# Performance work log

Hardware: AMD Instinct MI355X
Metric: run time of the kernel (lower is better)

Reference implementation:

```python
import jax, jax.numpy as jnp
import numpy as np
from jax import lax

N = 100000
G = 256          # voxel grid extent per axis
MULT = 8
C_HID = 32 * MULT  # 256
K3 = 27


def setup_inputs() -> dict:
    key = jax.random.key(0)
    k_feat, k1, k2, k3, k4 = jax.random.split(key, 5)
    # unique voxel coordinates in a G^3 grid (sparse tensors have no duplicate coords)
    rng = np.random.default_rng(0)
    lin = rng.choice(G * G * G, size=N, replace=False)
    coords = np.stack([lin // (G * G), (lin // G) % G, lin % G], axis=1).astype(np.int32)
    feats = jax.random.normal(k_feat, (N, 2), dtype=jnp.float32)
    def w(k, cin, cout):
        return jax.random.normal(k, (K3, cin, cout), dtype=jnp.float32) / np.sqrt(K3 * cin)
    return {
        "coords": jnp.asarray(coords),
        "feats": feats,
        "W1": w(k1, 2, C_HID),
        "W2": w(k2, C_HID, C_HID),
        "W3": w(k3, C_HID, C_HID),
        "W4": w(k4, C_HID, 2),
    }


def _neighbor_map(coords):
    """Kernel map for a 3x3x3 stride-1 sparse conv: for each of 27 offsets and each
    point i, the index j of the point at coords[i]+offset (and a validity mask).
    Built once and shared by all four layers (stride=1 preserves coordinates)."""
    S = G + 2  # pad linearization base so offsets in {-1,0,1} never wrap
    c = coords.astype(jnp.int32) + 1
    keys = (c[:, 0] * S + c[:, 1]) * S + c[:, 2]            # [N]
    order = jnp.argsort(keys)
    skeys = keys[order]
    offs = jnp.array([[dx, dy, dz] for dx in (-1, 0, 1)
                      for dy in (-1, 0, 1) for dz in (-1, 0, 1)], dtype=jnp.int32)  # [27,3]
    nc = c[None, :, :] + offs[:, None, :]                    # [27,N,3]
    qk = (nc[..., 0] * S + nc[..., 1]) * S + nc[..., 2]      # [27,N]
    pos = jnp.clip(jnp.searchsorted(skeys, qk), 0, N - 1)
    valid = skeys[pos] == qk                                 # [27,N]
    idx = order[pos]                                         # [27,N]
    return idx, valid


def _sparse_conv(feats, W, idx, valid):
    """gather -> GEMM -> accumulate, scanned over the 27 kernel offsets."""
    out0 = jnp.zeros((feats.shape[0], W.shape[-1]), feats.dtype)
    def step(acc, kv):
        i, v, w = kv
        g = jnp.where(v[:, None], feats[i], 0.0)   # [N,Cin] gathered neighbor feats
        return acc + g @ w, None
    out, _ = lax.scan(step, out0, (idx, valid, W))
    return out


def reference(coords, feats, W1, W2, W3, W4):
    idx, valid = _neighbor_map(coords)
    x = _sparse_conv(feats, W1, idx, valid)
    x = _sparse_conv(x, W2, idx, valid)
    x = _sparse_conv(x, W3, idx, valid)
    x = _sparse_conv(x, W4, idx, valid)
    return x
```

## Files before the change

### kernel.cpp

```cpp
#include <hip/hip_runtime.h>

#define HASH_BITS 19
#define HASH_SIZE (1u << HASH_BITS)
#define HASH_MASK (HASH_SIZE - 1)
#define EMPTY64 0xFFFFFFFFFFFFFFFFull
#define CH 256
#define PCH 32
#define NREP 8
#define NSEG (27 * NREP)
#define SEGCAP 4096
#define BM_WORDS 536704

typedef __attribute__((ext_vector_type(8))) short short8;
typedef __attribute__((ext_vector_type(4))) float floatx4;
typedef unsigned long long ull;

__device__ __forceinline__ unsigned cvt_pk_bf16(float a, float b) {
    unsigned r;
    asm("v_cvt_pk_bf16_f32 %0, %1, %2" : "=v"(r) : "v"(a), "v"(b));
    return r;
}

__device__ inline void split8_pack(const float* xa, uint4& hv, uint4& lv) {
#pragma unroll
    for (int p = 0; p < 4; ++p) {
        unsigned hp = cvt_pk_bf16(xa[2 * p], xa[2 * p + 1]);
        float h0 = __uint_as_float(hp << 16);
        float h1 = __uint_as_float(hp & 0xFFFF0000u);
        unsigned lp = cvt_pk_bf16(xa[2 * p] - h0, xa[2 * p + 1] - h1);
        ((unsigned*)&hv)[p] = hp;
        ((unsigned*)&lv)[p] = lp;
    }
}

__global__ void hash_insert_k(const int* __restrict__ coords, int n,
                              ull* __restrict__ tbl, unsigned* __restrict__ keys,
                              unsigned* __restrict__ bm) {
    int i = blockIdx.x * blockDim.x + threadIdx.x;
    if (i >= n) return;
    unsigned cx = (unsigned)(coords[3 * i + 0] + 1);
    unsigned cy = (unsigned)(coords[3 * i + 1] + 1);
    unsigned cz = (unsigned)(coords[3 * i + 2] + 1);
    unsigned key = (cx * 258u + cy) * 258u + cz;
    keys[i] = key;
    atomicOr(&bm[key >> 5], 1u << (key & 31));
    ull e = ((ull)key << 32) | (unsigned)i;
    unsigned h = (key * 2654435761u) & HASH_MASK;
    while (true) {
        ull prev = atomicCAS(&tbl[h], EMPTY64, e);
        if (prev == EMPTY64) return;
        h = (h + 1) & HASH_MASK;
    }
}

__global__ void neighbor_bm_k(const unsigned* __restrict__ keys, int n,
                              const unsigned* __restrict__ bm,
                              const ull* __restrict__ tbl,
                              int2* __restrict__ buckets, int* __restrict__ kcnt) {
    int t = blockIdx.x * blockDim.x + threadIdx.x;
    if (t >= n * 9) return;
    int rep = blockIdx.x & (NREP - 1);
    int i = t / 9, r = t - i * 9;
    unsigned key = keys[i];
    int base = (int)key + ((r / 3 - 1) * 258 + (r % 3 - 1)) * 258;
    unsigned bA = base - 1, bB = base, bC = base + 1;
    unsigned hit0 = (bm[bA >> 5] >> (bA & 31)) & 1u;
    unsigned hit1 = (bm[bB >> 5] >> (bB & 31)) & 1u;
    unsigned hit2 = (bm[bC >> 5] >> (bC & 31)) & 1u;
#pragma unroll
    for (int dz = -1; dz <= 1; ++dz) {
        if (r == 4 && dz == 0) continue;
        unsigned hit = dz < 0 ? hit0 : (dz == 0 ? hit1 : hit2);
        if (!hit) continue;
        unsigned nk = (unsigned)(base + dz);
        unsigned h = (nk * 2654435761u) & HASH_MASK;
        int j = -1;
        while (true) {
            ull e = tbl[h];
            if ((unsigned)(e >> 32) == nk) { j = (int)(e & 0xFFFFFFFFu); break; }
            if (e == EMPTY64) break;
            h = (h + 1) & HASH_MASK;
        }
        if (j >= 0) {
            int kk = 3 * r + dz + 1;
            int seg = kk * NREP + rep;
            int pos = atomicAdd(&kcnt[seg * 16], 1);
            buckets[(size_t)seg * SEGCAP + pos] = make_int2(i, j);
        }
    }
}

__global__ void chunk_desc_k(const int* __restrict__ kcnt,
                             int2* __restrict__ desc, int* __restrict__ nchunks) {
    __shared__ int cnts[NSEG];
    __shared__ int offs[NSEG + 1];
    int t = threadIdx.x;
    if (t < NSEG) cnts[t] = kcnt[t * 16];
    __syncthreads();
    if (t == 0) {
        int acc = 0;
        for (int s = 0; s < NSEG; ++s) { offs[s] = acc; acc += (cnts[s] + PCH - 1) / PCH; }
        offs[NSEG] = acc;
        *nchunks = acc;
    }
    __syncthreads();
    if (t < NSEG) {
        int cnt = cnts[t];
        int o = offs[t];
        int k = t / NREP;
        for (int c = 0; c * PCH < cnt; ++c) {
            int len = min(PCH, cnt - c * PCH);
            desc[o + c] = make_int2(t * SEGCAP + c * PCH, (k << 8) | len);
        }
    }
}

__global__ void prep_w_all_k(const float* __restrict__ W2, const float* __restrict__ W3,
                             unsigned short* __restrict__ Whi2, unsigned short* __restrict__ Wlo2,
                             unsigned short* __restrict__ Whi3, unsigned short* __restrict__ Wlo3) {
    int t = blockIdx.x * 256 + threadIdx.x;
    const int HALF = 27 * 8 * 256;
    if (t >= 2 * HALF) return;
    const float* W = (t < HALF) ? W2 : W3;
    unsigned short* Whi = (t < HALF) ? Whi2 : Whi3;
    unsigned short* Wlo = (t < HALF) ? Wlo2 : Wlo3;
    int tt = (t < HALF) ? t : t - HALF;
    int cout = tt & 255, kk = (tt >> 8) & 7, k = tt >> 11;
    int nt = cout >> 4, lc = cout & 15;
    const float* src = W + (size_t)k * 65536 + (size_t)kk * 32 * 256 + cout;
    size_t dbase = (((size_t)(k * 8 + kk) * 16 + nt) * 64 + lc) * 8;
#pragma unroll
    for (int kg = 0; kg < 4; ++kg) {
        float xa[8];
#pragma unroll
        for (int j = 0; j < 8; ++j) xa[j] = src[(size_t)(kg * 8 + j) * 256];
        uint4 hv, lv;
        split8_pack(xa, hv, lv);
        *(uint4*)(Whi + dbase + (size_t)kg * 16 * 8) = hv;
        *(uint4*)(Wlo + dbase + (size_t)kg * 16 * 8) = lv;
    }
}

__global__ void dense1_k(const float* __restrict__ x, const float* __restrict__ Wc,
                         float* __restrict__ out, int n) {
    int t = blockIdx.x * blockDim.x + threadIdx.x;
    if (t >= n * CH) return;
    int i = t >> 8, co = t & 255;
    float2 xv = *reinterpret_cast<const float2*>(x + 2 * i);
    out[t] = fmaf(xv.x, Wc[co], xv.y * Wc[CH + co]);
}

__global__ void sparse1b_k(const float* __restrict__ feats, const float* __restrict__ W1,
                           float* __restrict__ out, const int2* __restrict__ buckets,
                           const int2* __restrict__ desc, const int* __restrict__ nchunks) {
    __shared__ float xs[PCH][2];
    __shared__ int ii[PCH];
    int nc = *nchunks;
    int t = threadIdx.x;
    for (int m = blockIdx.x; m < nc; m += gridDim.x) {
        int2 d = desc[m];
        int k = d.y >> 8, len = d.y & 255;
        if (t < PCH) {
            if (t < len) {
                int2 pr = buckets[d.x + t];
                ii[t] = pr.x;
                xs[t][0] = feats[2 * pr.y];
                xs[t][1] = feats[2 * pr.y + 1];
            } else {
                ii[t] = -1;
                xs[t][0] = 0.f; xs[t][1] = 0.f;
            }
        }
        __syncthreads();
        const float* Wk = W1 + (size_t)k * 2 * CH;
        float w0 = Wk[t], w1 = Wk[CH + t];
#pragma unroll
        for (int p = 0; p < PCH; ++p) {
            int i = ii[p];
            if (i >= 0) atomicAdd(&out[(size_t)i * CH + t], fmaf(xs[p][0], w0, xs[p][1] * w1));
        }
        __syncthreads();
    }
}

__global__ __launch_bounds__(256) void dense_mid_mfma_k(
        const float* __restrict__ x,
        const unsigned short* __restrict__ Whi,
        const unsigned short* __restrict__ Wlo,
        float* __restrict__ out, int n) {
    __shared__ unsigned short AsH[8][2048];
    __shared__ unsigned short AsL[8][2048];
    int t = threadIdx.x;
    int wid = t >> 6, lane = t & 63;
    int i0 = blockIdx.x * 64;

    int row = ((t >> 6) << 4) + (t & 15);
    int kg = (t >> 4) & 3;
    float sok = (i0 + row < n) ? 1.f : 0.f;
    const float* sp = x + (size_t)min(i0 + row, n - 1) * CH + kg * 8;
#pragma unroll
    for (int kk = 0; kk < 8; ++kk) {
        floatx4 v0 = *(const floatx4*)(sp + kk * 32);
        floatx4 v1 = *(const floatx4*)(sp + kk * 32 + 4);
        float xa[8];
        xa[0] = v0.x * sok; xa[1] = v0.y * sok; xa[2] = v0.z * sok; xa[3] = v0.w * sok;
        xa[4] = v1.x * sok; xa[5] = v1.y * sok; xa[6] = v1.z * sok; xa[7] = v1.w * sok;
        uint4 hv, lv;
        split8_pack(xa, hv, lv);
        *(uint4*)&AsH[kk][t * 8] = hv;
        *(uint4*)&AsL[kk][t * 8] = lv;
    }
    __syncthreads();

    floatx4 acc[4][4];
#pragma unroll
    for (int a = 0; a < 4; ++a)
#pragma unroll
        for (int b = 0; b < 4; ++b) acc[a][b] = floatx4{0.f, 0.f, 0.f, 0.f};

    short8 Bh[2][4], Bl[2][4];
    auto loadB = [&](int kk, int b) {
#pragma unroll
        for (int q = 0; q < 4; ++q) {
            size_t off = (((size_t)kk * 16 + wid * 4 + q) * 64 + lane) * 8;
            Bh[b][q] = *(const short8*)&Whi[off];
            Bl[b][q] = *(const short8*)&Wlo[off];
        }
    };

    loadB(0, 0);
#pragma unroll
    for (int kk = 0; kk < 8; ++kk) {
        if (kk < 7) loadB(kk + 1, (kk + 1) & 1);
        int b = kk & 1;
#pragma unroll
        for (int mt = 0; mt < 4; ++mt) {
            short8 ah = *(const short8*)&AsH[kk][(mt * 64 + lane) * 8];
            short8 al = *(const short8*)&AsL[kk][(mt * 64 + lane) * 8];
#pragma unroll
            for (int q = 0; q < 4; ++q) {
                acc[mt][q] = __builtin_amdgcn_mfma_f32_16x16x32_bf16(ah, Bh[b][q], acc[mt][q], 0, 0, 0);
                acc[mt][q] = __builtin_amdgcn_mfma_f32_16x16x32_bf16(al, Bh[b][q], acc[mt][q], 0, 0, 0);
                acc[mt][q] = __builtin_amdgcn_mfma_f32_16x16x32_bf16(ah, Bl[b][q], acc[mt][q], 0, 0, 0);
            }
        }
    }

    int r0 = (lane >> 4) * 4, c0 = lane & 15;
#pragma unroll
    for (int mt = 0; mt < 4; ++mt)
#pragma unroll
        for (int r = 0; r < 4; ++r) {
            int orow = i0 + mt * 16 + r0 + r;
            if (orow < n) {
#pragma unroll
                for (int q = 0; q < 4; ++q)
                    out[(size_t)orow * CH + wid * 64 + q * 16 + c0] = acc[mt][q][r];
            }
        }
}

__global__ __launch_bounds__(256) void sparse_mid_mfma_k(
        const float* __restrict__ x,
        const unsigned short* __restrict__ Whi,
        const unsigned short* __restrict__ Wlo,
        float* __restrict__ out, const int2* __restrict__ buckets,
        const int2* __restrict__ desc, const int* __restrict__ nchunks) {
    __shared__ unsigned short As_hi[8192];
    __shared__ unsigned short As_lo[8192];
    __shared__ int ii[PCH];
    int nc = *nchunks;
    int t = threadIdx.x;
    int wid = t >> 6, lane = t & 63;
    int r = t >> 3, kk0 = t & 7;
    int mt_s = r >> 4, rl = r & 15;
    for (int m = blockIdx.x; m < nc; m += gridDim.x) {
        int2 d = desc[m];
        int k = d.y >> 8, len = d.y & 255;
        if (r < len) {
            int2 pr = buckets[d.x + r];
            if (kk0 == 0) ii[r] = pr.x;
            const float* src = x + (size_t)pr.y * CH + kk0 * 32;
#pragma unroll
            for (int kg = 0; kg < 4; ++kg) {
                float xa[8];
                floatx4 v0 = *(const floatx4*)(src + kg * 8);
                floatx4 v1 = *(const floatx4*)(src + kg * 8 + 4);
                xa[0] = v0.x; xa[1] = v0.y; xa[2] = v0.z; xa[3] = v0.w;
                xa[4] = v1.x; xa[5] = v1.y; xa[6] = v1.z; xa[7] = v1.w;
                uint4 hv, lv;
                split8_pack(xa, hv, lv);
                int ab = ((kk0 * 2 + mt_s) * 64 + kg * 16 + rl) * 8;
                *(uint4*)&As_hi[ab] = hv;
                *(uint4*)&As_lo[ab] = lv;
            }
        } else {
            if (kk0 == 0) ii[r] = -1;
            uint4 z = {0, 0, 0, 0};
#pragma unroll
            for (int kg = 0; kg < 4; ++kg) {
                int ab = ((kk0 * 2 + mt_s) * 64 + kg * 16 + rl) * 8;
                *(uint4*)&As_hi[ab] = z;
                *(uint4*)&As_lo[ab] = z;
            }
        }
        __syncthreads();
        floatx4 acc[2][4];
#pragma unroll
        for (int a = 0; a < 2; ++a)
#pragma unroll
            for (int b = 0; b < 4; ++b) acc[a][b] = floatx4{0.f, 0.f, 0.f, 0.f};

        short8 bh[2][4], bl[2][4];
        auto loadBs = [&](int kk, int b) {
#pragma unroll
            for (int q = 0; q < 4; ++q) {
                size_t off = (((size_t)(k * 8 + kk) * 16 + wid * 4 + q) * 64 + lane) * 8;
                bh[b][q] = *(const short8*)&Whi[off];
                bl[b][q] = *(const short8*)&Wlo[off];
            }
        };
        loadBs(0, 0);
#pragma unroll
        for (int kk = 0; kk < 8; ++kk) {
            if (kk < 7) loadBs(kk + 1, (kk + 1) & 1);
            int b = kk & 1;
            short8 ah0 = *(const short8*)&As_hi[((kk * 2 + 0) * 64 + lane) * 8];
            short8 al0 = *(const short8*)&As_lo[((kk * 2 + 0) * 64 + lane) * 8];
            short8 ah1 = *(const short8*)&As_hi[((kk * 2 + 1) * 64 + lane) * 8];
            short8 al1 = *(const short8*)&As_lo[((kk * 2 + 1) * 64 + lane) * 8];
#pragma unroll
            for (int q = 0; q < 4; ++q) {
                acc[0][q] = __builtin_amdgcn_mfma_f32_16x16x32_bf16(ah0, bh[b][q], acc[0][q], 0, 0, 0);
                acc[0][q] = __builtin_amdgcn_mfma_f32_16x16x32_bf16(al0, bh[b][q], acc[0][q], 0, 0, 0);
                acc[0][q] = __builtin_amdgcn_mfma_f32_16x16x32_bf16(ah0, bl[b][q], acc[0][q], 0, 0, 0);
                acc[1][q] = __builtin_amdgcn_mfma_f32_16x16x32_bf16(ah1, bh[b][q], acc[1][q], 0, 0, 0);
                acc[1][q] = __builtin_amdgcn_mfma_f32_16x16x32_bf16(al1, bh[b][q], acc[1][q], 0, 0, 0);
                acc[1][q] = __builtin_amdgcn_mfma_f32_16x16x32_bf16(ah1, bl[b][q], acc[1][q], 0, 0, 0);
            }
        }
        int r0 = (lane >> 4) * 4, c0 = lane & 15;
#pragma unroll
        for (int mt = 0; mt < 2; ++mt)
#pragma unroll
            for (int rr = 0; rr < 4; ++rr) {
                int orow = mt * 16 + r0 + rr;
                int i = ii[orow];
                if (i >= 0) {
#pragma unroll
                    for (int q = 0; q < 4; ++q)
                        atomicAdd(&out[(size_t)i * CH + wid * 64 + q * 16 + c0], acc[mt][q][rr]);
                }
            }
        __syncthreads();
    }
}

__device__ inline float wave_sum(float v) {
    for (int off = 32; off; off >>= 1) v += __shfl_xor(v, off);
    return v;
}

__global__ void dense4_k(const float* __restrict__ x, const float* __restrict__ Wc,
                         float* __restrict__ out, int n) {
    int wid = threadIdx.x >> 6, lane = threadIdx.x & 63;
    int i = blockIdx.x * 4 + wid;
    if (i >= n) return;
    floatx4 xv = *reinterpret_cast<const floatx4*>(x + (size_t)i * CH + lane * 4);
    floatx4 w0 = *reinterpret_cast<const floatx4*>(Wc + lane * 8);
    floatx4 w1 = *reinterpret_cast<const floatx4*>(Wc + lane * 8 + 4);
    float a0 = xv.x * w0.x + xv.y * w0.z + xv.z * w1.x + xv.w * w1.z;
    float a1 = xv.x * w0.y + xv.y * w0.w + xv.z * w1.y + xv.w * w1.w;
    a0 = wave_sum(a0);
    a1 = wave_sum(a1);
    if (lane == 0) { out[2 * i] = a0; out[2 * i + 1] = a1; }
}

__global__ void sparse4b_k(const float* __restrict__ x, const float* __restrict__ W4,
                           float* __restrict__ out, const int2* __restrict__ buckets,
                           const int2* __restrict__ desc, const int* __restrict__ nchunks) {
    int nc = *nchunks;
    int wid = threadIdx.x >> 6, lane = threadIdx.x & 63;
    for (int m = blockIdx.x; m < nc; m += gridDim.x) {
        int2 d = desc[m];
        int k = d.y >> 8, len = d.y & 255;
        const float* Wk = W4 + (size_t)k * CH * 2;
        floatx4 w0 = *reinterpret_cast<const floatx4*>(Wk + lane * 8);
        floatx4 w1 = *reinterpret_cast<const floatx4*>(Wk + lane * 8 + 4);
        for (int p = wid; p < len; p += 4) {
            int2 pr = buckets[d.x + p];
            floatx4 xv = *reinterpret_cast<const floatx4*>(x + (size_t)pr.y * CH + lane * 4);
            float a0 = xv.x * w0.x + xv.y * w0.z + xv.z * w1.x + xv.w * w1.z;
            float a1 = xv.x * w0.y + xv.y * w0.w + xv.z * w1.y + xv.w * w1.w;
            a0 = wave_sum(a0);
            a1 = wave_sum(a1);
            if (lane == 0) {
                atomicAdd(&out[2 * pr.x], a0);
                atomicAdd(&out[2 * pr.x + 1], a1);
            }
        }
    }
}

extern "C" void kernel_launch(void* const* d_in, const int* in_sizes, int n_in,
                              void* d_out, int out_size, void* d_ws, size_t ws_size,
                              hipStream_t stream) {
    const int* coords = (const int*)d_in[0];
    const float* feats = (const float*)d_in[1];
    const float* W1 = (const float*)d_in[2];
    const float* W2 = (const float*)d_in[3];
    const float* W3 = (const float*)d_in[4];
    const float* W4 = (const float*)d_in[5];
    float* out = (float*)d_out;
    int n = in_sizes[0] / 3;

    char* ws = (char*)d_ws;
    auto alloc = [&](size_t bytes) -> void* {
        void* p = (void*)ws;
        ws += (bytes + 255) & ~(size_t)255;
        return p;
    };
    ull* tbl = (ull*)alloc((size_t)HASH_SIZE * 8);
    unsigned* bm = (unsigned*)alloc((size_t)BM_WORDS * 4);
    int* kcnt = (int*)alloc((size_t)NSEG * 16 * 4);
    unsigned* keys = (unsigned*)alloc((size_t)n * 4);
    int* nchunks = (int*)alloc(4);
    int ndesc = NSEG * (SEGCAP / PCH);
    int2* desc = (int2*)alloc(sizeof(int2) * (size_t)ndesc);
    int2* buckets = (int2*)alloc(sizeof(int2) * (size_t)NSEG * SEGCAP);
    unsigned short* Whi2 = (unsigned short*)alloc((size_t)27 * 65536 * 2);
    unsigned short* Wlo2 = (unsigned short*)alloc((size_t)27 * 65536 * 2);
    unsigned short* Whi3 = (unsigned short*)alloc((size_t)27 * 65536 * 2);
    unsigned short* Wlo3 = (unsigned short*)alloc((size_t)27 * 65536 * 2);
    float* x1 = (float*)alloc((size_t)n * CH * 4);
    float* x2 = (float*)alloc((size_t)n * CH * 4);

    hipMemsetAsync(tbl, 0xFF, (size_t)HASH_SIZE * 8, stream);
    hipMemsetAsync(bm, 0, (size_t)BM_WORDS * 4 + (size_t)NSEG * 16 * 4, stream);

    hash_insert_k<<<(n + 255) / 256, 256, 0, stream>>>(coords, n, tbl, keys, bm);
    neighbor_bm_k<<<(n * 9 + 255) / 256, 256, 0, stream>>>(keys, n, bm, tbl, buckets, kcnt);
    chunk_desc_k<<<1, 256, 0, stream>>>(kcnt, desc, nchunks);
    prep_w_all_k<<<(2 * 27 * 8 * 256) / 256, 256, 0, stream>>>(W2, W3, Whi2, Wlo2, Whi3, Wlo3);

    int mtiles = (n + 63) / 64;

    dense1_k<<<(n * CH + 255) / 256, 256, 0, stream>>>(feats, W1 + 13 * 2 * CH, x1, n);
    sparse1b_k<<<1024, 256, 0, stream>>>(feats, W1, x1, buckets, desc, nchunks);

    dense_mid_mfma_k<<<mtiles, 256, 0, stream>>>(x1, Whi2 + (size_t)13 * 65536,
                                                 Wlo2 + (size_t)13 * 65536, x2, n);
    sparse_mid_mfma_k<<<512, 256, 0, stream>>>(x1, Whi2, Wlo2, x2, buckets, desc, nchunks);

    dense_mid_mfma_k<<<mtiles, 256, 0, stream>>>(x2, Whi3 + (size_t)13 * 65536,
                                                 Wlo3 + (size_t)13 * 65536, x1, n);
    sparse_mid_mfma_k<<<512, 256, 0, stream>>>(x2, Whi3, Wlo3, x1, buckets, desc, nchunks);

    dense4_k<<<(n + 3) / 4, 256, 0, stream>>>(x1, W4 + 13 * CH * 2, out, n);
    sparse4b_k<<<512, 256, 0, stream>>>(x1, W4, out, buckets, desc, nchunks);
}
```

Measured before the change: 301.6 us.

## Pipeline A-tile staging through triple-buffered LDS in dense mid-layer MFMA kernel

The dense mid-layer GEMM kernel stops staging all eight K-slices of the activation tile into shared memory before computing. It now keeps a three-slot ring, prefetching the next slice's global loads while MFMAs run on the current slice, and sets launch bounds to ask for three blocks per SM. This shrinks LDS per block from 64KB to 24KB to raise occupancy and overlap global-load latency with compute. In exchange it adds a barrier per K step and some register pressure.

```diff
diff --git a/kernel.cpp b/kernel.cpp
--- a/kernel.cpp
+++ b/kernel.cpp
@@ -183,42 +183,30 @@
     }
 }
 
-__global__ __launch_bounds__(256) void dense_mid_mfma_k(
+__global__ __launch_bounds__(256, 3) void dense_mid_mfma_k(
         const float* __restrict__ x,
         const unsigned short* __restrict__ Whi,
         const unsigned short* __restrict__ Wlo,
         float* __restrict__ out, int n) {
-    __shared__ unsigned short AsH[8][2048];
-    __shared__ unsigned short AsL[8][2048];
+    __shared__ unsigned short AsH[3][2048], AsL[3][2048];
     int t = threadIdx.x;
     int wid = t >> 6, lane = t & 63;
     int i0 = blockIdx.x * 64;
+
+    floatx4 acc[4][4];
+#pragma unroll
+    for (int a = 0; a < 4; ++a)
+#pragma unroll
+        for (int b = 0; b < 4; ++b) acc[a][b] = floatx4{0.f, 0.f, 0.f, 0.f};
 
     int row = ((t >> 6) << 4) + (t & 15);
     int kg = (t >> 4) & 3;
     float sok = (i0 + row < n) ? 1.f : 0.f;
     const float* sp = x + (size_t)min(i0 + row, n - 1) * CH + kg * 8;
-#pragma unroll
-    for (int kk = 0; kk < 8; ++kk) {
-        floatx4 v0 = *(const floatx4*)(sp + kk * 32);
-        floatx4 v1 = *(const floatx4*)(sp + kk * 32 + 4);
-        float xa[8];
-        xa[0] = v0.x * sok; xa[1] = v0.y * sok; xa[2] = v0.z * sok; xa[3] = v0.w * sok;
-        xa[4] = v1.x * sok; xa[5] = v1.y * sok; xa[6] = v1.z * sok; xa[7] = v1.w * sok;
-        uint4 hv, lv;
-        split8_pack(xa, hv, lv);
-        *(uint4*)&AsH[kk][t * 8] = hv;
-        *(uint4*)&AsL[kk][t * 8] = lv;
-    }
-    __syncthreads();
-
-    floatx4 acc[4][4];
-#pragma unroll
-    for (int a = 0; a < 4; ++a)
-#pragma unroll
-        for (int b = 0; b < 4; ++b) acc[a][b] = floatx4{0.f, 0.f, 0.f, 0.f};
-
+
+    floatx4 ra0, ra1;
     short8 Bh[2][4], Bl[2][4];
+
     auto loadB = [&](int kk, int b) {
 #pragma unroll
         for (int q = 0; q < 4; ++q) {
@@ -227,16 +215,24 @@
             Bl[b][q] = *(const short8*)&Wlo[off];
         }
     };
-
-    loadB(0, 0);
-#pragma unroll
-    for (int kk = 0; kk < 8; ++kk) {
-        if (kk < 7) loadB(kk + 1, (kk + 1) & 1);
-        int b = kk & 1;
+    auto loadA = [&](int kk) {
+        ra0 = *(const floatx4*)(sp + kk * 32);
+        ra1 = *(const floatx4*)(sp + kk * 32 + 4);
+    };
+    auto writeA = [&](int bi) {
+        float xa[8];
+        xa[0] = ra0.x * sok; xa[1] = ra0.y * sok; xa[2] = ra0.z * sok; xa[3] = ra0.w * sok;
+        xa[4] = ra1.x * sok; xa[5] = ra1.y * sok; xa[6] = ra1.z * sok; xa[7] = ra1.w * sok;
+        uint4 hv, lv;
+        split8_pack(xa, hv, lv);
+        *(uint4*)&AsH[bi][t * 8] = hv;
+        *(uint4*)&AsL[bi][t * 8] = lv;
+    };
+    auto compute = [&](int bi, int b) {
 #pragma unroll
         for (int mt = 0; mt < 4; ++mt) {
-            short8 ah = *(const short8*)&AsH[kk][(mt * 64 + lane) * 8];
-            short8 al = *(const short8*)&AsL[kk][(mt * 64 + lane) * 8];
+            short8 ah = *(const short8*)&AsH[bi][(mt * 64 + lane) * 8];
+            short8 al = *(const short8*)&AsL[bi][(mt * 64 + lane) * 8];
 #pragma unroll
             for (int q = 0; q < 4; ++q) {
                 acc[mt][q] = __builtin_amdgcn_mfma_f32_16x16x32_bf16(ah, Bh[b][q], acc[mt][q], 0, 0, 0);
@@ -244,6 +240,20 @@
                 acc[mt][q] = __builtin_amdgcn_mfma_f32_16x16x32_bf16(ah, Bl[b][q], acc[mt][q], 0, 0, 0);
             }
         }
+    };
+
+    loadB(0, 0);
+    loadA(0); writeA(0);
+    loadA(1); writeA(1);
+    __syncthreads();
+
+#pragma unroll
+    for (int kk = 0; kk < 8; ++kk) {
+        if (kk < 7) loadB(kk + 1, (kk + 1) & 1);
+        if (kk < 6) loadA(kk + 2);
+        compute(kk % 3, kk & 1);
+        if (kk < 6) writeA((kk + 2) % 3);
+        __syncthreads();
     }
 
     int r0 = (lane >> 4) * 4, c0 = lane & 15;
```

New measurement: 282.2 us. 6.5% less time.
